# Kernel tuning notes

Measured on AMD Instinct MI355X. Metric: run time of the kernel, lower is better.

## Reference

```python
import jax, jax.numpy as jnp
import numpy as np

N = 100000   # nodes
F = 128      # feature len
E = 1600000  # edges per graph (avg degree 16)


def setup_inputs() -> dict:
    key = jax.random.key(0)
    ks = jax.random.split(key, 32)
    def nrm(k, shape, scale=0.05):
        return jax.random.normal(k, shape, jnp.float32) * scale
    inp = {"X": jax.random.normal(ks[0], (N, F), jnp.float32)}
    i = 1
    for g in (1, 2, 3):
        inp[f"edge_index{g}"] = jax.random.randint(ks[i], (2, E), 0, N, dtype=jnp.int32); i += 1
        inp[f"edge_weight{g}"] = jax.random.uniform(ks[i], (E,), jnp.float32); i += 1
        inp[f"g{g}_w1"] = nrm(ks[i], (F, F)); i += 1
        inp[f"g{g}_b1"] = jnp.zeros((F,), jnp.float32)
        inp[f"g{g}_w2"] = nrm(ks[i], (F, F)); i += 1
        inp[f"g{g}_b2"] = jnp.zeros((F,), jnp.float32)
    for name in ("fc1", "fc2"):
        inp[f"{name}_w1"] = nrm(ks[i], (F, 256)); i += 1
        inp[f"{name}_b1"] = jnp.zeros((256,), jnp.float32)
        inp[f"{name}_w2"] = nrm(ks[i], (256, 128)); i += 1
        inp[f"{name}_b2"] = jnp.zeros((128,), jnp.float32)
        inp[f"{name}_w3"] = nrm(ks[i], (128, 64)); i += 1
        inp[f"{name}_b3"] = jnp.zeros((64,), jnp.float32)
    return inp


def gcn_conv(x, w, b, src, dst, ew):
    # PyG GCNConv: add self-loops (weight 1), symmetric normalization.
    n = x.shape[0]
    h = x @ w                                                   # [N, F]
    deg = jax.ops.segment_sum(ew, dst, num_segments=n) + 1.0    # [N]
    dinv = jax.lax.rsqrt(deg)
    norm = dinv[src] * ew * dinv[dst]                           # [E]
    agg = jax.ops.segment_sum(h[src] * norm[:, None], dst, num_segments=n)
    agg = agg + (dinv * dinv)[:, None] * h                      # self-loop term
    return agg + b


def single_module(x, src, dst, ew, w1, b1, w2, b2):
    x = jax.nn.relu(gcn_conv(x, w1, b1, src, dst, ew))
    x = jax.nn.relu(gcn_conv(x, w2, b2, src, dst, ew))
    return x


def fc_layer(x, w1, b1, w2, b2, w3, b3):
    x = jax.nn.relu(x @ w1 + b1)
    x = jax.nn.relu(x @ w2 + b2)
    return jax.nn.relu(x @ w3 + b3)


def reference(X, edge_index1, edge_weight1, g1_w1, g1_b1, g1_w2, g1_b2,
              edge_index2, edge_weight2, g2_w1, g2_b1, g2_w2, g2_b2,
              edge_index3, edge_weight3, g3_w1, g3_b1, g3_w2, g3_b2,
              fc1_w1, fc1_b1, fc1_w2, fc1_b2, fc1_w3, fc1_b3,
              fc2_w1, fc2_b1, fc2_w2, fc2_b2, fc2_w3, fc2_b3):
    X0 = fc_layer(X, fc1_w1, fc1_b1, fc1_w2, fc1_b2, fc1_w3, fc1_b3)
    X1 = single_module(X, edge_index1[0], edge_index1[1], edge_weight1, g1_w1, g1_b1, g1_w2, g1_b2)
    X1 = fc_layer(X1, fc2_w1, fc2_b1, fc2_w2, fc2_b2, fc2_w3, fc2_b3)
    X2 = single_module(X, edge_index2[0], edge_index2[1], edge_weight2, g2_w1, g2_b1, g2_w2, g2_b2)
    X2 = fc_layer(X2, fc2_w1, fc2_b1, fc2_w2, fc2_b2, fc2_w3, fc2_b3)
    X3 = single_module(X, edge_index3[0], edge_index3[1], edge_weight3, g3_w1, g3_b1, g3_w2, g3_b2)
    X3 = fc_layer(X3, fc2_w1, fc2_b1, fc2_w2, fc2_b2, fc2_w3, fc2_b3)
    Xs = X0 + X1 + X2 + X3
    return (Xs, X1, X2, X3)
```

## Files before the change

### kernel.cpp

```cpp
#include <hip/hip_runtime.h>


typedef short bf16x8 __attribute__((ext_vector_type(8)));
typedef float f32x4 __attribute__((ext_vector_type(4)));

#define BSHIFT 8
#define NBUCK_MAX 400
#define BCAP 6144
#define WDSCALE 8388608.f

static __device__ __forceinline__ float frelu(float x) { return x > 0.f ? x : 0.f; }

static __device__ __forceinline__ unsigned short f2bf(float f) {
    unsigned int u = __float_as_uint(f);
    u += 0x7fffu + ((u >> 16) & 1u);
    return (unsigned short)(u >> 16);
}
static __device__ __forceinline__ float bflo(unsigned int u) {
    return __uint_as_float(u << 16);
}
static __device__ __forceinline__ float bfhi(unsigned int u) {
    return __uint_as_float(u & 0xffff0000u);
}

__global__ void xconv(const float* __restrict__ src, unsigned short* __restrict__ dst, int n4) {
    int i = blockIdx.x * 256 + threadIdx.x;
    if (i >= n4) return;
    float4 v = *(const float4*)(src + (size_t)i * 4);
    ushort4 o = {f2bf(v.x), f2bf(v.y), f2bf(v.z), f2bf(v.w)};
    *(ushort4*)(dst + (size_t)i * 4) = o;
}

__global__ void wtrans(const float* __restrict__ src, unsigned short* __restrict__ dst,
                       int K, int M) {
    int i = blockIdx.x * 256 + threadIdx.x;
    if (i >= K * M) return;
    int m = i / K, k = i % K;
    dst[i] = f2bf(src[(size_t)k * M + m]);
}

__global__ void zero_small(int* __restrict__ p, int n) {
    int i = blockIdx.x * 256 + threadIdx.x;
    if (i < n) p[i] = 0;
}

__global__ __launch_bounds__(256) void part_k(
    const int* __restrict__ src, const int* __restrict__ dst,
    const float* __restrict__ ew, int* __restrict__ gcur,
    int2* __restrict__ part, int nE, int nbuck) {
    __shared__ int lh[NBUCK_MAX];
    __shared__ int gb[NBUCK_MAX];
    const int tid = threadIdx.x;
    for (int t = tid; t < nbuck; t += 256) lh[t] = 0;
    __syncthreads();
    const int e0 = blockIdx.x * 4096;
    int rk[16], bk[16];
#pragma unroll
    for (int j = 0; j < 16; ++j) {
        int e = e0 + j * 256 + tid;
        rk[j] = -1;
        if (e < nE) {
            int b = dst[e] >> BSHIFT;
            bk[j] = b;
            rk[j] = atomicAdd(&lh[b], 1);
        }
    }
    __syncthreads();
    for (int t = tid; t < nbuck; t += 256)
        gb[t] = lh[t] ? atomicAdd(&gcur[t], lh[t]) : 0;
    __syncthreads();
#pragma unroll
    for (int j = 0; j < 16; ++j) {
        int e = e0 + j * 256 + tid;
        if (e >= nE) continue;
        int b = bk[j];
        int slot = gb[b] + rk[j];
        if (slot >= 0 && slot < BCAP) {
            int s = src[e];
            int dl = dst[e] & ((1 << BSHIFT) - 1);
            part[(size_t)b * BCAP + slot] = make_int2(s | (dl << 17), __float_as_int(ew[e]));
        }
    }
}

__global__ void scanB(const int* __restrict__ gcur, int* __restrict__ bbase,
                      int* __restrict__ rp, int n, int nbuck) {
    __shared__ int s[512];
    int t = threadIdx.x;
    int c = (t < nbuck) ? gcur[t] : 0;
    if (c > BCAP) c = BCAP;
    s[t] = c;
    __syncthreads();
#pragma unroll
    for (int off = 1; off < 512; off <<= 1) {
        int x = (t >= off) ? s[t - off] : 0;
        __syncthreads();
        s[t] += x;
        __syncthreads();
    }
    if (t < nbuck) bbase[t] = s[t] - c;
    if (t == nbuck - 1) rp[n] = s[t];
}

__global__ __launch_bounds__(256) void csr_bucket(
    const int2* __restrict__ part, const int* __restrict__ gcur,
    const int* __restrict__ bbase, int2* __restrict__ ev,
    int* __restrict__ rp, float* __restrict__ dinv, int n) {
    __shared__ int hist[256];
    __shared__ int cur[256];
    __shared__ int wd[256];
    const int b = blockIdx.x;
    const int t = threadIdx.x;
    int cnt = gcur[b];
    if (cnt > BCAP) cnt = BCAP;
    const int gbase = bbase[b];
    const int2* pb = part + (size_t)b * BCAP;

    hist[t] = 0; wd[t] = 0;
    __syncthreads();
    for (int i = t; i < cnt; i += 256)
        atomicAdd(&hist[(pb[i].x >> 17) & 255], 1);
    __syncthreads();
    int myh = hist[t];
#pragma unroll
    for (int off = 1; off < 256; off <<= 1) {
        int x = (t >= off) ? hist[t - off] : 0;
        __syncthreads();
        hist[t] += x;
        __syncthreads();
    }
    int excl = hist[t] - myh;
    cur[t] = excl;
    __syncthreads();
    for (int i = t; i < cnt; i += 256) {
        int2 p = pb[i];
        int dl = (p.x >> 17) & 255;
        int pos = atomicAdd(&cur[dl], 1);
        ev[(size_t)gbase + pos] = make_int2(p.x & 0x1FFFF, p.y);
        atomicAdd(&wd[dl], (int)(__int_as_float(p.y) * WDSCALE + 0.5f));
    }
    __syncthreads();
    int g = (b << BSHIFT) + t;
    if (g < n) {
        dinv[g] = rsqrtf(1.f + (float)wd[t] * (1.f / WDSCALE));
        rp[g] = gbase + excl;
    }
}

__global__ __launch_bounds__(256) void gather_bf(
    const int* __restrict__ rp, const int2* __restrict__ ev,
    const unsigned short* __restrict__ h,
    const float* __restrict__ dinv, const float* __restrict__ bias,
    unsigned short* __restrict__ aggr, int n) {
    int node = (int)(((size_t)blockIdx.x * 256 + threadIdx.x) >> 6);
    if (node >= n) return;
    int lane = threadIdx.x & 63;
    float di = dinv[node];
    float sl = di * di;
    unsigned int hu = *(const unsigned int*)(h + (size_t)node * 128 + lane * 2);
    float2 bv = *(const float2*)(bias + lane * 2);
    float a0x = 0.f, a0y = 0.f, a1x = 0.f, a1y = 0.f;
    float a2x = 0.f, a2y = 0.f, a3x = 0.f, a3y = 0.f;
    int beg = rp[node], end = rp[node + 1];
    int i = beg;
    for (; i + 3 < end; i += 4) {
        int2 e0 = ev[i], e1 = ev[i + 1], e2 = ev[i + 2], e3 = ev[i + 3];
        float n0 = dinv[e0.x] * __int_as_float(e0.y);
        float n1 = dinv[e1.x] * __int_as_float(e1.y);
        float n2 = dinv[e2.x] * __int_as_float(e2.y);
        float n3 = dinv[e3.x] * __int_as_float(e3.y);
        unsigned int u0 = *(const unsigned int*)(h + (size_t)e0.x * 128 + lane * 2);
        unsigned int u1 = *(const unsigned int*)(h + (size_t)e1.x * 128 + lane * 2);
        unsigned int u2 = *(const unsigned int*)(h + (size_t)e2.x * 128 + lane * 2);
        unsigned int u3 = *(const unsigned int*)(h + (size_t)e3.x * 128 + lane * 2);
        a0x += n0 * bflo(u0); a0y += n0 * bfhi(u0);
        a1x += n1 * bflo(u1); a1y += n1 * bfhi(u1);
        a2x += n2 * bflo(u2); a2y += n2 * bfhi(u2);
        a3x += n3 * bflo(u3); a3y += n3 * bfhi(u3);
    }
    for (; i < end; ++i) {
        int2 e0 = ev[i];
        float n0 = dinv[e0.x] * __int_as_float(e0.y);
        unsigned int u0 = *(const unsigned int*)(h + (size_t)e0.x * 128 + lane * 2);
        a0x += n0 * bflo(u0); a0y += n0 * bfhi(u0);
    }
    float ox = frelu(di * ((a0x + a1x) + (a2x + a3x)) + sl * bflo(hu) + bv.x);
    float oy = frelu(di * ((a0y + a1y) + (a2y + a3y)) + sl * bfhi(hu) + bv.y);
    unsigned int o = (unsigned int)f2bf(ox) | ((unsigned int)f2bf(oy) << 16);
    *(unsigned int*)(aggr + (size_t)node * 128 + lane * 2) = o;
}

template<int K, int BN, int RELU, int EPI>
__global__ __launch_bounds__(256, 2) void gemm_bf(
    const unsigned short* __restrict__ A, const unsigned short* __restrict__ Wt,
    const float* __restrict__ bias, void* __restrict__ Cout,
    int M, int nrows, float* __restrict__ xs) {
    constexpr int BM = 128, BK = 64;
    constexpr int WN = BN / 2;
    constexpr int NF = WN / 16;
    static_assert(BN == 64 || BN == 128, "BN");
    __shared__ unsigned short As[BM][BK + 8];
    __shared__ unsigned short Bs[BN][BK + 8];

    const int tid  = threadIdx.x;
    const int wid  = tid >> 6;
    const int lane = tid & 63;
    const int wm   = (wid >> 1) * 64;
    const int wn   = (wid & 1) * WN;
    const int row0 = blockIdx.x * BM;
    const int col0 = blockIdx.y * BN;
    const int lr   = lane & 15;
    const int lk   = (lane >> 4) * 8;

    f32x4 acc[4][NF] = {};

    for (int k0 = 0; k0 < K; k0 += BK) {
#pragma unroll
        for (int it = 0; it < 4; ++it) {
            int f = tid + it * 256;
            int r = f >> 3, g = f & 7;
            int grow = row0 + r;
            if (grow >= nrows) grow = nrows - 1;
            bf16x8 v = *(const bf16x8*)(A + (size_t)grow * K + k0 + g * 8);
            *(bf16x8*)&As[r][g * 8] = v;
        }
#pragma unroll
        for (int it = 0; it < BN / 32; ++it) {
            int f = tid + it * 256;
            int nidx = f >> 3, g = f & 7;
            bf16x8 v = *(const bf16x8*)(Wt + (size_t)(col0 + nidx) * K + k0 + g * 8);
            *(bf16x8*)&Bs[nidx][g * 8] = v;
        }
        __syncthreads();
#pragma unroll
        for (int kk = 0; kk < 2; ++kk) {
            bf16x8 af[4], bfv[NF];
#pragma unroll
            for (int mi = 0; mi < 4; ++mi)
                af[mi] = *(const bf16x8*)&As[wm + 16 * mi + lr][kk * 32 + lk];
#pragma unroll
            for (int ni = 0; ni < NF; ++ni)
                bfv[ni] = *(const bf16x8*)&Bs[wn + 16 * ni + lr][kk * 32 + lk];
#pragma unroll
            for (int mi = 0; mi < 4; ++mi)
#pragma unroll
                for (int ni = 0; ni < NF; ++ni)
                    acc[mi][ni] = __builtin_amdgcn_mfma_f32_16x16x32_bf16(
                        af[mi], bfv[ni], acc[mi][ni], 0, 0, 0);
        }
        __syncthreads();
    }

    const int dr0 = (lane >> 4) * 4;
#pragma unroll
    for (int ni = 0; ni < NF; ++ni) {
        int col = col0 + wn + 16 * ni + lr;
        float bv = bias ? bias[col] : 0.f;
#pragma unroll
        for (int mi = 0; mi < 4; ++mi) {
#pragma unroll
            for (int r = 0; r < 4; ++r) {
                int grow = row0 + wm + 16 * mi + dr0 + r;
                if (grow >= nrows) continue;
                float v = acc[mi][ni][r] + bv;
                if (RELU) v = frelu(v);
                if (EPI == 0) {
                    ((unsigned short*)Cout)[(size_t)grow * M + col] = f2bf(v);
                } else {
                    ((float*)Cout)[(size_t)grow * M + col] = v;
                    if (EPI == 2) xs[(size_t)grow * 64 + col] += v;
                }
            }
        }
    }
}

extern "C" void kernel_launch(void* const* d_in, const int* in_sizes, int n_in,
                              void* d_out, int out_size, void* d_ws, size_t ws_size,
                              hipStream_t stream) {
    (void)n_in; (void)out_size; (void)ws_size;
    const float* X = (const float*)d_in[0];
    const int N = in_sizes[0] / 128;

    const float* fc1_w1 = (const float*)d_in[19];
    const float* fc1_b1 = (const float*)d_in[20];
    const float* fc1_w2 = (const float*)d_in[21];
    const float* fc1_b2 = (const float*)d_in[22];
    const float* fc1_w3 = (const float*)d_in[23];
    const float* fc1_b3 = (const float*)d_in[24];
    const float* fc2_w1 = (const float*)d_in[25];
    const float* fc2_b1 = (const float*)d_in[26];
    const float* fc2_w2 = (const float*)d_in[27];
    const float* fc2_b2 = (const float*)d_in[28];
    const float* fc2_w3 = (const float*)d_in[29];
    const float* fc2_b3 = (const float*)d_in[30];

    float* out = (float*)d_out;
    float* Xs  = out;

    char* base = (char*)d_ws;
    const size_t Npad = (((size_t)N + 255) / 256) * 256;
    float*          dinv  = (float*)base;                 base += Npad * 4;
    unsigned short* Xbf   = (unsigned short*)base;        base += (size_t)N * 128 * 2;
    unsigned short* t1bf  = (unsigned short*)base;        base += (size_t)N * 256 * 2;
    unsigned short* t2bf  = (unsigned short*)base;        base += (size_t)N * 128 * 2;
    unsigned short* aggbf = (unsigned short*)base;        base += (size_t)N * 128 * 2;
    unsigned short* wtbuf = (unsigned short*)base;

    unsigned short* fc1w1t = wtbuf;
    unsigned short* fc1w2t = fc1w1t + 32768;
    unsigned short* fc1w3t = fc1w2t + 32768;
    unsigned short* fc2w1t = fc1w3t + 8192;
    unsigned short* fc2w2t = fc2w1t + 32768;
    unsigned short* fc2w3t = fc2w2t + 32768;
    unsigned short* gwt    = fc2w3t + 8192;

    const dim3 blk(256);
    const int GR = (N + 127) / 128;
    const int NBUCK = (N + 255) >> 8;
    const int GWB = (int)(((size_t)N * 64 + 255) / 256);

    xconv<<<(N * 32 + 255) / 256, blk, 0, stream>>>(X, Xbf, N * 32);
    wtrans<<<(128 * 256 + 255) / 256, blk, 0, stream>>>(fc1_w1, fc1w1t, 128, 256);
    wtrans<<<(256 * 128 + 255) / 256, blk, 0, stream>>>(fc1_w2, fc1w2t, 256, 128);
    wtrans<<<(128 * 64 + 255) / 256, blk, 0, stream>>>(fc1_w3, fc1w3t, 128, 64);
    wtrans<<<(128 * 256 + 255) / 256, blk, 0, stream>>>(fc2_w1, fc2w1t, 128, 256);
    wtrans<<<(256 * 128 + 255) / 256, blk, 0, stream>>>(fc2_w2, fc2w2t, 256, 128);
    wtrans<<<(128 * 64 + 255) / 256, blk, 0, stream>>>(fc2_w3, fc2w3t, 128, 64);
    for (int g = 0; g < 3; ++g) {
        wtrans<<<(128 * 128 + 255) / 256, blk, 0, stream>>>(
            (const float*)d_in[3 + 6 * g], gwt + g * 32768, 128, 128);
        wtrans<<<(128 * 128 + 255) / 256, blk, 0, stream>>>(
            (const float*)d_in[5 + 6 * g], gwt + g * 32768 + 16384, 128, 128);
    }

    gemm_bf<128, 128, 1, 0><<<dim3(GR, 2), blk, 0, stream>>>(Xbf, fc1w1t, fc1_b1, t1bf, 256, N, nullptr);
    gemm_bf<256, 128, 1, 0><<<dim3(GR, 1), blk, 0, stream>>>(t1bf, fc1w2t, fc1_b2, t2bf, 128, N, nullptr);
    gemm_bf<128, 64, 1, 1><<<dim3(GR, 1), blk, 0, stream>>>(t2bf, fc1w3t, fc1_b3, Xs, 64, N, nullptr);

    for (int g = 0; g < 3; ++g) {
        const int*   ei  = (const int*)d_in[1 + 6 * g];
        const int    E   = in_sizes[1 + 6 * g] / 2;
        const int*   srp = ei;
        const int*   dsp = ei + E;
        const float* ew  = (const float*)d_in[2 + 6 * g];
        const float* b1  = (const float*)d_in[4 + 6 * g];
        const float* b2  = (const float*)d_in[6 + 6 * g];
        unsigned short* w1t = gwt + g * 32768;
        unsigned short* w2t = w1t + 16384;

        int2* part  = (int2*)t1bf;
        int2* ev    = part + (size_t)NBUCK * BCAP;
        int*  rpn   = (int*)(ev + E);
        int*  gcur  = rpn + (N + 1);
        int*  bbase = gcur + NBUCK;

        zero_small<<<(NBUCK + 255) / 256, blk, 0, stream>>>(gcur, NBUCK);
        part_k<<<(E + 4095) / 4096, blk, 0, stream>>>(srp, dsp, ew, gcur, part, E, NBUCK);
        scanB<<<1, 512, 0, stream>>>(gcur, bbase, rpn, N, NBUCK);
        csr_bucket<<<NBUCK, blk, 0, stream>>>(part, gcur, bbase, ev, rpn, dinv, N);

        gemm_bf<128, 128, 0, 0><<<dim3(GR, 1), blk, 0, stream>>>(Xbf, w1t, nullptr, t2bf, 128, N, nullptr);
        gather_bf<<<GWB, blk, 0, stream>>>(rpn, ev, t2bf, dinv, b1, aggbf, N);
        gemm_bf<128, 128, 0, 0><<<dim3(GR, 1), blk, 0, stream>>>(aggbf, w2t, nullptr, t2bf, 128, N, nullptr);
        gather_bf<<<GWB, blk, 0, stream>>>(rpn, ev, t2bf, dinv, b2, aggbf, N);

        gemm_bf<128, 128, 1, 0><<<dim3(GR, 2), blk, 0, stream>>>(aggbf, fc2w1t, fc2_b1, t1bf, 256, N, nullptr);
        gemm_bf<256, 128, 1, 0><<<dim3(GR, 1), blk, 0, stream>>>(t1bf, fc2w2t, fc2_b2, t2bf, 128, N, nullptr);
        gemm_bf<128, 64, 1, 2><<<dim3(GR, 1), blk, 0, stream>>>(
            t2bf, fc2w3t, fc2_b3, out + (size_t)(1 + g) * N * 64, 64, N, Xs);
    }
}
```

Baseline: 1.133 ms.

## Gather four edges per wavefront with 16-byte loads; swap GEMM grid axes

The gather kernel now splits each 64-lane wavefront into four 16-lane groups. Each group handles a different edge and loads 8 bf16 features per lane with one uint4 load, and the partial sums are combined with cross-lane xor shuffles. This aims to raise memory-level parallelism and use wider, fewer loads on the random neighbour-row fetches, at the cost of shuffle reductions and idle lanes on the tail iteration. Separately, the GEMM grids are transposed so the column-tile index comes from blockIdx.x, which places the two N-tiles of the same row block next to each other in launch order for better A-tile cache reuse.

Result: slower. 1.195 ms (+5.5%).

```diff
diff --git a/kernel.cpp b/kernel.cpp
--- a/kernel.cpp
+++ b/kernel.cpp
@@ -154,40 +154,50 @@
     unsigned short* __restrict__ aggr, int n) {
     int node = (int)(((size_t)blockIdx.x * 256 + threadIdx.x) >> 6);
     if (node >= n) return;
-    int lane = threadIdx.x & 63;
-    float di = dinv[node];
-    float sl = di * di;
-    unsigned int hu = *(const unsigned int*)(h + (size_t)node * 128 + lane * 2);
-    float2 bv = *(const float2*)(bias + lane * 2);
-    float a0x = 0.f, a0y = 0.f, a1x = 0.f, a1y = 0.f;
-    float a2x = 0.f, a2y = 0.f, a3x = 0.f, a3y = 0.f;
-    int beg = rp[node], end = rp[node + 1];
-    int i = beg;
-    for (; i + 3 < end; i += 4) {
-        int2 e0 = ev[i], e1 = ev[i + 1], e2 = ev[i + 2], e3 = ev[i + 3];
-        float n0 = dinv[e0.x] * __int_as_float(e0.y);
-        float n1 = dinv[e1.x] * __int_as_float(e1.y);
-        float n2 = dinv[e2.x] * __int_as_float(e2.y);
-        float n3 = dinv[e3.x] * __int_as_float(e3.y);
-        unsigned int u0 = *(const unsigned int*)(h + (size_t)e0.x * 128 + lane * 2);
-        unsigned int u1 = *(const unsigned int*)(h + (size_t)e1.x * 128 + lane * 2);
-        unsigned int u2 = *(const unsigned int*)(h + (size_t)e2.x * 128 + lane * 2);
-        unsigned int u3 = *(const unsigned int*)(h + (size_t)e3.x * 128 + lane * 2);
-        a0x += n0 * bflo(u0); a0y += n0 * bfhi(u0);
-        a1x += n1 * bflo(u1); a1y += n1 * bfhi(u1);
-        a2x += n2 * bflo(u2); a2y += n2 * bfhi(u2);
-        a3x += n3 * bflo(u3); a3y += n3 * bfhi(u3);
-    }
-    for (; i < end; ++i) {
-        int2 e0 = ev[i];
-        float n0 = dinv[e0.x] * __int_as_float(e0.y);
-        unsigned int u0 = *(const unsigned int*)(h + (size_t)e0.x * 128 + lane * 2);
-        a0x += n0 * bflo(u0); a0y += n0 * bfhi(u0);
-    }
-    float ox = frelu(di * ((a0x + a1x) + (a2x + a3x)) + sl * bflo(hu) + bv.x);
-    float oy = frelu(di * ((a0y + a1y) + (a2y + a3y)) + sl * bfhi(hu) + bv.y);
-    unsigned int o = (unsigned int)f2bf(ox) | ((unsigned int)f2bf(oy) << 16);
-    *(unsigned int*)(aggr + (size_t)node * 128 + lane * 2) = o;
+    const int lane = threadIdx.x & 63;
+    const int grp  = lane >> 4;
+    const int fl   = lane & 15;
+
+    float acc[8];
+#pragma unroll
+    for (int j = 0; j < 8; ++j) acc[j] = 0.f;
+
+    const int beg = rp[node], end = rp[node + 1];
+    for (int i = beg; i < end; i += 4) {
+        int e = i + grp;
+        bool v = e < end;
+        int2 r = ev[v ? e : beg];
+        float nm = v ? dinv[r.x] * __int_as_float(r.y) : 0.f;
+        uint4 u = *(const uint4*)(h + (size_t)r.x * 128 + fl * 8);
+        acc[0] += nm * bflo(u.x); acc[1] += nm * bfhi(u.x);
+        acc[2] += nm * bflo(u.y); acc[3] += nm * bfhi(u.y);
+        acc[4] += nm * bflo(u.z); acc[5] += nm * bfhi(u.z);
+        acc[6] += nm * bflo(u.w); acc[7] += nm * bfhi(u.w);
+    }
+#pragma unroll
+    for (int j = 0; j < 8; ++j) acc[j] += __shfl_xor(acc[j], 16, 64);
+#pragma unroll
+    for (int j = 0; j < 8; ++j) acc[j] += __shfl_xor(acc[j], 32, 64);
+
+    if (grp == 0) {
+        float di = dinv[node];
+        float sl = di * di;
+        uint4 hu = *(const uint4*)(h + (size_t)node * 128 + fl * 8);
+        float4 b0 = *(const float4*)(bias + fl * 8);
+        float4 b1 = *(const float4*)(bias + fl * 8 + 4);
+        float hx[8] = {bflo(hu.x), bfhi(hu.x), bflo(hu.y), bfhi(hu.y),
+                       bflo(hu.z), bfhi(hu.z), bflo(hu.w), bfhi(hu.w)};
+        float bb[8] = {b0.x, b0.y, b0.z, b0.w, b1.x, b1.y, b1.z, b1.w};
+        unsigned int pk[4];
+#pragma unroll
+        for (int j = 0; j < 4; ++j) {
+            float o0 = frelu(di * acc[2 * j]     + sl * hx[2 * j]     + bb[2 * j]);
+            float o1 = frelu(di * acc[2 * j + 1] + sl * hx[2 * j + 1] + bb[2 * j + 1]);
+            pk[j] = (unsigned int)f2bf(o0) | ((unsigned int)f2bf(o1) << 16);
+        }
+        *(uint4*)(aggr + (size_t)node * 128 + fl * 8) =
+            make_uint4(pk[0], pk[1], pk[2], pk[3]);
+    }
 }
 
 template<int K, int BN, int RELU, int EPI>
@@ -207,8 +217,8 @@
     const int lane = tid & 63;
     const int wm   = (wid >> 1) * 64;
     const int wn   = (wid & 1) * WN;
-    const int row0 = blockIdx.x * BM;
-    const int col0 = blockIdx.y * BN;
+    const int row0 = blockIdx.y * BM;
+    const int col0 = blockIdx.x * BN;
     const int lr   = lane & 15;
     const int lk   = (lane >> 4) * 8;
 
@@ -334,9 +344,9 @@
             (const float*)d_in[5 + 6 * g], gwt + g * 32768 + 16384, 128, 128);
     }
 
-    gemm_bf<128, 128, 1, 0><<<dim3(GR, 2), blk, 0, stream>>>(Xbf, fc1w1t, fc1_b1, t1bf, 256, N, nullptr);
-    gemm_bf<256, 128, 1, 0><<<dim3(GR, 1), blk, 0, stream>>>(t1bf, fc1w2t, fc1_b2, t2bf, 128, N, nullptr);
-    gemm_bf<128, 64, 1, 1><<<dim3(GR, 1), blk, 0, stream>>>(t2bf, fc1w3t, fc1_b3, Xs, 64, N, nullptr);
+    gemm_bf<128, 128, 1, 0><<<dim3(2, GR), blk, 0, stream>>>(Xbf, fc1w1t, fc1_b1, t1bf, 256, N, nullptr);
+    gemm_bf<256, 128, 1, 0><<<dim3(1, GR), blk, 0, stream>>>(t1bf, fc1w2t, fc1_b2, t2bf, 128, N, nullptr);
+    gemm_bf<128, 64, 1, 1><<<dim3(1, GR), blk, 0, stream>>>(t2bf, fc1w3t, fc1_b3, Xs, 64, N, nullptr);
 
     for (int g = 0; g < 3; ++g) {
         const int*   ei  = (const int*)d_in[1 + 6 * g];
@@ -360,14 +370,14 @@
         scanB<<<1, 512, 0, stream>>>(gcur, bbase, rpn, N, NBUCK);
         csr_bucket<<<NBUCK, blk, 0, stream>>>(part, gcur, bbase, ev, rpn, dinv, N);
 
-        gemm_bf<128, 128, 0, 0><<<dim3(GR, 1), blk, 0, stream>>>(Xbf, w1t, nullptr, t2bf, 128, N, nullptr);
+        gemm_bf<128, 128, 0, 0><<<dim3(1, GR), blk, 0, stream>>>(Xbf, w1t, nullptr, t2bf, 128, N, nullptr);
         gather_bf<<<GWB, blk, 0, stream>>>(rpn, ev, t2bf, dinv, b1, aggbf, N);
-        gemm_bf<128, 128, 0, 0><<<dim3(GR, 1), blk, 0, stream>>>(aggbf, w2t, nullptr, t2bf, 128, N, nullptr);
+        gemm_bf<128, 128, 0, 0><<<dim3(1, GR), blk, 0, stream>>>(aggbf, w2t, nullptr, t2bf, 128, N, nullptr);
         gather_bf<<<GWB, blk, 0, stream>>>(rpn, ev, t2bf, dinv, b2, aggbf, N);
 
-        gemm_bf<128, 128, 1, 0><<<dim3(GR, 2), blk, 0, stream>>>(aggbf, fc2w1t, fc2_b1, t1bf, 256, N, nullptr);
-        gemm_bf<256, 128, 1, 0><<<dim3(GR, 1), blk, 0, stream>>>(t1bf, fc2w2t, fc2_b2, t2bf, 128, N, nullptr);
-        gemm_bf<128, 64, 1, 2><<<dim3(GR, 1), blk, 0, stream>>>(
+        gemm_bf<128, 128, 1, 0><<<dim3(2, GR), blk, 0, stream>>>(aggbf, fc2w1t, fc2_b1, t1bf, 256, N, nullptr);
+        gemm_bf<256, 128, 1, 0><<<dim3(1, GR), blk, 0, stream>>>(t1bf, fc2w2t, fc2_b2, t2bf, 128, N, nullptr);
+        gemm_bf<128, 64, 1, 2><<<dim3(1, GR), blk, 0, stream>>>(
             t2bf, fc2w3t, fc2_b3, out + (size_t)(1 + g) * N * 64, 64, N, Xs);
     }
 }
```
